# Kernel optimization log

Measured on AMD Instinct MI355X. Metric: run time of the kernel, lower is better.

Reference implementation:

```python
import jax, jax.numpy as jnp
import numpy as np

B, L = 4096, 200
G_DIM, L_DIM, A_DIM, H = 64, 64, 8, 32
MAX_ACTION = 1.0


def _init(k, shape, fan_in):
    bound = 1.0 / np.sqrt(fan_in)
    return jax.random.uniform(k, shape, jnp.float32, -bound, bound)


def setup_inputs() -> dict:
    key = jax.random.key(0)
    ks = jax.random.split(key, 16)
    return dict(
        global_states=jax.random.normal(ks[0], (B, G_DIM), jnp.float32),
        local_states=jax.random.normal(ks[1], (B, L, L_DIM), jnp.float32),
        W_w=_init(ks[2], (H, G_DIM), G_DIM), W_b=_init(ks[3], (H,), G_DIM),
        U_w=_init(ks[4], (H, L_DIM), L_DIM), U_b=_init(ks[5], (H,), L_DIM),
        att_w=_init(ks[6], (1, 2 * H), 2 * H), att_b=_init(ks[7], (1,), 2 * H),
        l1_w=_init(ks[8], (256, 2 * H), 2 * H), l1_b=_init(ks[9], (256,), 2 * H),
        l2_w=_init(ks[10], (256, 256), 256), l2_b=_init(ks[11], (256,), 256),
        l3_w=_init(ks[12], (A_DIM, 256), 256), l3_b=_init(ks[13], (A_DIM,), 256),
    )


def reference(global_states, local_states, W_w, W_b, U_w, U_b,
              att_w, att_b, l1_w, l1_b, l2_w, l2_b, l3_w, l3_b):
    h = W_w.shape[0]  # 32
    wg = global_states @ W_w.T + W_b                              # [B,H]
    ul = jnp.einsum('bld,hd->blh', local_states, U_w) + U_b       # [B,L,H]
    # att input row0 = cat(wg, wg); rows 1..L = cat(wg, ul)
    a_g, a_l = att_w[0, :h], att_w[0, h:]
    g_term = wg @ a_g                                             # [B]
    s0 = jax.nn.leaky_relu(g_term + wg @ a_l + att_b[0])          # [B]
    sl = jax.nn.leaky_relu(g_term[:, None] + ul @ a_l + att_b[0]) # [B,L]
    # normalize by sum (not softmax), matching torch.div(score, score.sum())
    total = s0 + sl.sum(axis=1)                                   # [B]
    n0 = s0 / total                                               # [B]
    nl = sl / total[:, None]                                      # [B,L]
    agg_local = jnp.einsum('bl,blh->bh', nl, ul)                  # [B,H]
    states = jax.nn.relu(jnp.concatenate([n0[:, None] * wg, agg_local], axis=1))  # [B,2H]
    a = jax.nn.relu(states @ l1_w.T + l1_b)
    a = jax.nn.relu(a @ l2_w.T + l2_b)
    a = jax.nn.sigmoid(a @ l3_w.T + l3_b)
    return MAX_ACTION * a
```

## Files before the change

kernel.cpp:

```cpp
#include <hip/hip_runtime.h>
#include <math.h>

#define BB 4096
#define LL 200
#define HH 32
#define PF 8


template<int CTRL>
__device__ __forceinline__ float dpp_ror_add(float x)
{
    int y = __builtin_amdgcn_update_dpp(0, __float_as_int(x),
                                        CTRL, 0xF, 0xF, true);
    return x + __int_as_float(y);
}

__global__ __launch_bounds__(256) void actor_fused_kernel(
    const float* __restrict__ gs,
    const float* __restrict__ ls,
    const float* __restrict__ W_w, const float* __restrict__ W_b,
    const float* __restrict__ U_w, const float* __restrict__ U_b,
    const float* __restrict__ att_w, const float* __restrict__ att_b,
    const float* __restrict__ l1_w, const float* __restrict__ l1_b,
    const float* __restrict__ l2_w, const float* __restrict__ l2_b,
    const float* __restrict__ l3_w, const float* __restrict__ l3_b,
    float* __restrict__ out)
{
    __shared__ float c_lds[4 * 64];
    __shared__ float y_lds[4 * 64];
    __shared__ __align__(16) float s_x [4 * 64];
    __shared__ __align__(16) float s_a1[4 * 256];
    __shared__ __align__(16) float s_a2[4 * 260];

    const int tid  = threadIdx.x;
    const int lane = tid & 63;
    const int wid  = tid >> 6;
    const int b    = blockIdx.x * 4 + wid;

    const int h    = lane & 31;
    const int half = lane >> 5;
    const int q    = lane & 15;
    const int lg   = lane >> 4;


    const float4* g4 = (const float4*)(gs + (size_t)b * 64);
    const float4* W4 = (const float4*)(W_w);
    float wg = (half == 0) ? W_b[h] : 0.f;
    #pragma unroll
    for (int dd = 0; dd < 8; ++dd) {
        float4 gv = g4[half * 8 + dd];
        float4 wv = W4[h * 16 + half * 8 + dd];
        wg += gv.x * wv.x + gv.y * wv.y + gv.z * wv.z + gv.w * wv.w;
    }
    wg += __shfl_xor(wg, 32);

    float gt = wg * att_w[h];
    float t2 = wg * att_w[HH + h];
    #pragma unroll
    for (int m = 1; m < 32; m <<= 1) {
        gt += __shfl_xor(gt, m);
        t2 += __shfl_xor(t2, m);
    }
    const float attb = att_b[0];
    const float lin0 = gt + t2 + attb;
    const float s0   = (lin0 > 0.f) ? lin0 : 0.01f * lin0;

    float c = 0.f;
    float ubal = 0.f;
    #pragma unroll
    for (int hh = 0; hh < HH; ++hh) {
        const float alh = att_w[HH + hh];
        c    += alh * U_w[hh * 64 + lane];
        ubal += alh * U_b[hh];
    }
    c_lds[wid * 64 + lane] = c;
    __syncthreads();
    const float4 cq = *(const float4*)&c_lds[wid * 64 + 4 * q];
    const float base = gt + ubal + attb;

    const float4* xs = (const float4*)(ls + (size_t)b * (LL * 64));
    const int idx0 = lg * 16 + q;
    float4 yx = make_float4(0.f, 0.f, 0.f, 0.f);
    float Sacc = 0.f;

    float4 Xbuf[PF];
    #pragma unroll
    for (int i = 0; i < PF; ++i)
        Xbuf[i] = xs[idx0 + i * 64];

    #pragma unroll
    for (int t = 0; t < 50; ++t) {
        float4 X = Xbuf[t & (PF - 1)];
        int tn = t + PF;
        if (tn > 49) tn = 49;
        Xbuf[t & (PF - 1)] = xs[idx0 + tn * 64];

        float p = X.x * cq.x + X.y * cq.y + X.z * cq.z + X.w * cq.w;
        p = dpp_ror_add<0x121>(p);
        p = dpp_ror_add<0x122>(p);
        p = dpp_ror_add<0x124>(p);
        p = dpp_ror_add<0x128>(p);
        const float linv = p + base;
        const float sl = (linv > 0.f) ? linv : 0.01f * linv;
        yx.x += sl * X.x;
        yx.y += sl * X.y;
        yx.z += sl * X.z;
        yx.w += sl * X.w;
        Sacc += sl;
    }

    #pragma unroll
    for (int m = 16; m < 64; m <<= 1) {
        yx.x += __shfl_xor(yx.x, m);
        yx.y += __shfl_xor(yx.y, m);
        yx.z += __shfl_xor(yx.z, m);
        yx.w += __shfl_xor(yx.w, m);
        Sacc += __shfl_xor(Sacc, m);
    }
    if (lane < 16) *(float4*)&y_lds[wid * 64 + 4 * q] = yx;
    __syncthreads();

    float V = (half == 0) ? (U_b[h] * Sacc) : 0.f;
    const float4* U4 = (const float4*)U_w;
    const float4* y4 = (const float4*)&y_lds[wid * 64];
    #pragma unroll
    for (int dd = 0; dd < 8; ++dd) {
        float4 uv = U4[h * 16 + half * 8 + dd];
        float4 yv = y4[half * 8 + dd];
        V += uv.x * yv.x + uv.y * yv.y + uv.z * yv.z + uv.w * yv.w;
    }
    V += __shfl_xor(V, 32);

    const float total = s0 + Sacc;
    const float n0    = s0 / total;
    const float outv  = (lane < 32) ? (n0 * wg) : (V / total);
    s_x[wid * 64 + lane] = fmaxf(outv, 0.f);
    __syncthreads();


    float w[64];

    {
        const float* wr = l1_w + tid * 64;
        #pragma unroll
        for (int d = 0; d < 64; ++d) w[d] = wr[d];
        float bias = l1_b[tid];
        #pragma unroll
        for (int r = 0; r < 4; ++r) {
            float acc = bias;
            #pragma unroll
            for (int d = 0; d < 64; ++d)
                acc += s_x[r * 64 + d] * w[d];
            s_a1[r * 256 + tid] = fmaxf(acc, 0.f);
        }
    }
    __syncthreads();

    {
        float acc[4];
        float bias = l2_b[tid];
        #pragma unroll
        for (int r = 0; r < 4; ++r) acc[r] = bias;
        for (int kc = 0; kc < 4; ++kc) {
            const float* wr = l2_w + tid * 256 + kc * 64;
            #pragma unroll
            for (int d = 0; d < 64; ++d) w[d] = wr[d];
            #pragma unroll
            for (int r = 0; r < 4; ++r) {
                #pragma unroll
                for (int d = 0; d < 64; ++d)
                    acc[r] += s_a1[r * 256 + kc * 64 + d] * w[d];
            }
        }
        #pragma unroll
        for (int r = 0; r < 4; ++r)
            s_a2[r * 260 + tid] = fmaxf(acc[r], 0.f);
    }
    __syncthreads();

    if (tid < 32) {
        int r = tid >> 3, o = tid & 7;
        float acc = l3_b[o];
        const float4* wr4 = (const float4*)(l3_w + o * 256);
        const float4* a4  = (const float4*)&s_a2[r * 260];
        #pragma unroll 8
        for (int k = 0; k < 64; ++k) {
            float4 av = a4[k];
            float4 wv = wr4[k];
            acc += av.x * wv.x + av.y * wv.y + av.z * wv.z + av.w * wv.w;
        }
        out[(size_t)(blockIdx.x * 4 + r) * 8 + o] =
            1.f / (1.f + __expf(-acc));
    }
}

extern "C" void kernel_launch(void* const* d_in, const int* in_sizes, int n_in,
                              void* d_out, int out_size, void* d_ws, size_t ws_size,
                              hipStream_t stream)
{
    const float* gs    = (const float*)d_in[0];
    const float* ls    = (const float*)d_in[1];
    const float* W_w   = (const float*)d_in[2];
    const float* W_b   = (const float*)d_in[3];
    const float* U_w   = (const float*)d_in[4];
    const float* U_b   = (const float*)d_in[5];
    const float* att_w = (const float*)d_in[6];
    const float* att_b = (const float*)d_in[7];
    const float* l1_w  = (const float*)d_in[8];
    const float* l1_b  = (const float*)d_in[9];
    const float* l2_w  = (const float*)d_in[10];
    const float* l2_b  = (const float*)d_in[11];
    const float* l3_w  = (const float*)d_in[12];
    const float* l3_b  = (const float*)d_in[13];

    actor_fused_kernel<<<BB / 4, 256, 0, stream>>>(
        gs, ls, W_w, W_b, U_w, U_b, att_w, att_b,
        l1_w, l1_b, l2_w, l2_b, l3_w, l3_b, (float*)d_out);
}
```

Baseline: 355.1 us.

## Restructure MLP layers to coalesced float4 weight loads with DPP row reductions

The l1 and l2 layers no longer have each thread own one output neuron and read a strided weight row. A 16-lane group now cooperates on one neuron: each lane loads a contiguous float4 slice of the weight row, forms partial dot products against activations held in registers, and reduces them with DPP row rotations. This gives coalesced weight reads and drops the large per-thread weight array and the repeated LDS reads. The cost is extra DPP reduction instructions and a write where only one lane in sixteen is active; s_a1 is padded to a stride of 260.

After: 352.9 us. Within noise of the previous version (-0.6%).

```diff
diff --git a/kernel.cpp b/kernel.cpp
--- a/kernel.cpp
+++ b/kernel.cpp
@@ -29,7 +29,7 @@
     __shared__ float c_lds[4 * 64];
     __shared__ float y_lds[4 * 64];
     __shared__ __align__(16) float s_x [4 * 64];
-    __shared__ __align__(16) float s_a1[4 * 256];
+    __shared__ __align__(16) float s_a1[4 * 260];
     __shared__ __align__(16) float s_a2[4 * 260];
 
     const int tid  = threadIdx.x;
@@ -137,44 +137,70 @@
     s_x[wid * 64 + lane] = fmaxf(outv, 0.f);
     __syncthreads();
 
-
-    float w[64];
+    const int kl  = lane & 15;
+    const int lgb = lane >> 4;
 
     {
-        const float* wr = l1_w + tid * 64;
-        #pragma unroll
-        for (int d = 0; d < 64; ++d) w[d] = wr[d];
-        float bias = l1_b[tid];
-        #pragma unroll
-        for (int r = 0; r < 4; ++r) {
-            float acc = bias;
-            #pragma unroll
-            for (int d = 0; d < 64; ++d)
-                acc += s_x[r * 64 + d] * w[d];
-            s_a1[r * 256 + tid] = fmaxf(acc, 0.f);
-        }
-    }
-    __syncthreads();
-
-    {
-        float acc[4];
-        float bias = l2_b[tid];
-        #pragma unroll
-        for (int r = 0; r < 4; ++r) acc[r] = bias;
-        for (int kc = 0; kc < 4; ++kc) {
-            const float* wr = l2_w + tid * 256 + kc * 64;
-            #pragma unroll
-            for (int d = 0; d < 64; ++d) w[d] = wr[d];
+        float4 xr[4];
+        #pragma unroll
+        for (int r = 0; r < 4; ++r)
+            xr[r] = *(const float4*)&s_x[r * 64 + kl * 4];
+
+        #pragma unroll
+        for (int i = 0; i < 16; ++i) {
+            const int u = (wid << 6) + (i << 2) + lgb;
+            const float4 wv = *(const float4*)(l1_w + u * 64 + kl * 4);
+            const float bias = l1_b[u];
             #pragma unroll
             for (int r = 0; r < 4; ++r) {
-                #pragma unroll
-                for (int d = 0; d < 64; ++d)
-                    acc[r] += s_a1[r * 256 + kc * 64 + d] * w[d];
+                float acc = wv.x * xr[r].x + wv.y * xr[r].y
+                          + wv.z * xr[r].z + wv.w * xr[r].w;
+                acc = dpp_ror_add<0x121>(acc);
+                acc = dpp_ror_add<0x122>(acc);
+                acc = dpp_ror_add<0x124>(acc);
+                acc = dpp_ror_add<0x128>(acc);
+                if (kl == 0)
+                    s_a1[r * 260 + u] = fmaxf(acc + bias, 0.f);
             }
         }
+    }
+    __syncthreads();
+
+    {
+        float4 a1r[4][4];
         #pragma unroll
         for (int r = 0; r < 4; ++r)
-            s_a2[r * 260 + tid] = fmaxf(acc[r], 0.f);
+            #pragma unroll
+            for (int s = 0; s < 4; ++s)
+                a1r[r][s] = *(const float4*)&s_a1[r * 260 + s * 64 + kl * 4];
+
+        #pragma unroll
+        for (int i = 0; i < 16; ++i) {
+            const int u = (wid << 6) + (i << 2) + lgb;
+            const float* wr = l2_w + (size_t)u * 256;
+            const float4 wv0 = *(const float4*)(wr +   0 + kl * 4);
+            const float4 wv1 = *(const float4*)(wr +  64 + kl * 4);
+            const float4 wv2 = *(const float4*)(wr + 128 + kl * 4);
+            const float4 wv3 = *(const float4*)(wr + 192 + kl * 4);
+            const float bias = l2_b[u];
+            #pragma unroll
+            for (int r = 0; r < 4; ++r) {
+                float acc = wv0.x * a1r[r][0].x + wv0.y * a1r[r][0].y
+                          + wv0.z * a1r[r][0].z + wv0.w * a1r[r][0].w;
+                acc      += wv1.x * a1r[r][1].x + wv1.y * a1r[r][1].y
+                          + wv1.z * a1r[r][1].z + wv1.w * a1r[r][1].w;
+                acc      += wv2.x * a1r[r][2].x + wv2.y * a1r[r][2].y
+                          + wv2.z * a1r[r][2].z + wv2.w * a1r[r][2].w;
+                acc      += wv3.x * a1r[r][3].x + wv3.y * a1r[r][3].y
+                          + wv3.z * a1r[r][3].z + wv3.w * a1r[r][3].w;
+                acc = dpp_ror_add<0x121>(acc);
+                acc = dpp_ror_add<0x122>(acc);
+                acc = dpp_ror_add<0x124>(acc);
+                acc = dpp_ror_add<0x128>(acc);
+                if (kl == 0)
+                    s_a2[r * 260 + u] = fmaxf(acc + bias, 0.f);
+            }
+        }
     }
     __syncthreads();
 
```
